# Optimization experiments

Hardware: AMD Instinct MI355X
Metric: run time of the kernel (lower is better)

Reference implementation:

```python
import jax, jax.numpy as jnp
import numpy as np

N_NODES = 50000
N_EDGES = 800000
D_IN = 128
D_OUT = 128


def setup_inputs() -> dict:
    key = jax.random.key(0)
    k_feat, k_src, k_dst, k_ws, k_bs, k_wn = jax.random.split(key, 6)
    feat = jax.random.normal(k_feat, (N_NODES, D_IN), dtype=jnp.float32)
    src = jax.random.randint(k_src, (N_EDGES,), 0, N_NODES, dtype=jnp.int64)
    dst = jax.random.randint(k_dst, (N_EDGES,), 0, N_NODES, dtype=jnp.int64)
    # fc_self: Linear(D_IN, D_OUT, bias=True); fc_neigh: Linear(D_IN, D_OUT, bias=False)
    W_self = jax.random.normal(k_ws, (D_OUT, D_IN), dtype=jnp.float32) * (1.0 / np.sqrt(D_IN))
    b_self = jax.random.normal(k_bs, (D_OUT,), dtype=jnp.float32) * 0.01
    # xavier_uniform with relu gain
    gain = float(np.sqrt(2.0))
    bound = gain * float(np.sqrt(6.0 / (D_IN + D_OUT)))
    W_neigh = jax.random.uniform(k_wn, (D_OUT, D_IN), dtype=jnp.float32, minval=-bound, maxval=bound)
    bias = jnp.zeros((D_OUT,), dtype=jnp.float32)
    return {"feat": feat, "src": src, "dst": dst, "W_self": W_self,
            "b_self": b_self, "W_neigh": W_neigh, "bias": bias}


def reference(feat, src, dst, W_self, b_self, W_neigh, bias):
    # copy_u('h','m') + fn.mean('m','neigh'): gather src feats, mean-reduce by dst.
    # lin_before_mp is False (in_feats == out_feats), so aggregate raw feats first.
    n = feat.shape[0]
    msgs = feat[src]                                             # [E, D_IN]
    neigh_sum = jax.ops.segment_sum(msgs, dst, num_segments=n)   # [N, D_IN]
    deg = jax.ops.segment_sum(jnp.ones(src.shape, feat.dtype), dst, num_segments=n)
    # DGL mean yields 0 for zero-in-degree nodes
    h_neigh = jnp.where(deg[:, None] > 0, neigh_sum / jnp.maximum(deg, 1.0)[:, None], 0.0)
    h_neigh = h_neigh @ W_neigh.T                                # fc_neigh (no bias)
    h_self = feat @ W_self.T + b_self                            # fc_self
    return h_self + h_neigh + bias
```

## Files before the change

kernel.cpp:

```cpp
#include <hip/hip_runtime.h>
#include <hip/hip_fp8.h>

#define N_NODES 50000
#define N_EDGES 800000
#define D 128
#define NBUK 782
#define CAPB 1344
#define SRTN (CAPB + 64*7)
#define EPB 2048
#define SCAT_BLOCKS 391
#define FEAT_BLOCKS 3125
#define W_BLOCKS 32
#define CAPC 16

typedef __bf16 bf16x8 __attribute__((ext_vector_type(8)));
typedef __bf16 bf16x4 __attribute__((ext_vector_type(4)));
typedef float  f32x4  __attribute__((ext_vector_type(4)));
typedef float  f32x2  __attribute__((ext_vector_type(2)));

#if defined(__has_builtin)
#if __has_builtin(__builtin_amdgcn_cvt_pk_f32_fp8) && __has_builtin(__builtin_amdgcn_cvt_pk_fp8_f32)
#define HW_FP8 1
#endif
#endif

#define OFF_PACKED 0ull
#define OFF_FEAT8  19568768ull
#define OFF_WC16   25968896ull
#define OFF_BIASC  26034432ull

__device__ __forceinline__ float fp8tof_sw(unsigned char b) {
    __hip_fp8_e4m3 t; t.__x = b;
    return (float)t;
}

__global__ __launch_bounds__(256)
void prep_kernel(const int* __restrict__ src, const int* __restrict__ dst,
                 int* __restrict__ packed,
                 const float* __restrict__ feat, unsigned char* __restrict__ feat8,
                 const float* __restrict__ Ws, const float* __restrict__ Wn,
                 const float* __restrict__ b_self, const float* __restrict__ bias,
                 __bf16* __restrict__ Wc16, float* __restrict__ biasc, int n) {
    const int tid = threadIdx.x;
    const int bid = blockIdx.x;
    if (bid < SCAT_BLOCKS) {
        __shared__ int hist[NBUK];
        __shared__ int boff[NBUK];
        __shared__ int srtL[EPB];
        __shared__ int wtot[4];
        const int e0 = bid * EPB;
        int d[8], s[8];
        for (int i = tid; i < NBUK; i += 256) hist[i] = 0;
        __syncthreads();
        #pragma unroll
        for (int j = 0; j < 8; ++j) {
            int e = e0 + j * 256 + tid;
            bool ok = e < n;
            d[j] = ok ? dst[e] : -1;
            s[j] = ok ? src[e] : 0;
            if (ok) atomicAdd(&hist[d[j] >> 6], 1);
        }
        __syncthreads();
        {
            const int lane = tid & 63;
            const int wv = tid >> 6;
            const int b4 = tid * 4;
            int h0 = (b4 + 0 < NBUK) ? hist[b4 + 0] : 0;
            int h1 = (b4 + 1 < NBUK) ? hist[b4 + 1] : 0;
            int h2 = (b4 + 2 < NBUK) ? hist[b4 + 2] : 0;
            int h3 = (b4 + 3 < NBUK) ? hist[b4 + 3] : 0;
            int sm = h0 + h1 + h2 + h3;
            int v = sm;
            #pragma unroll
            for (int o = 1; o < 64; o <<= 1) {
                int u = __shfl_up(v, o);
                if (lane >= o) v += u;
            }
            if (lane == 63) wtot[wv] = v;
            __syncthreads();
            if (tid == 0) {
                int r = 0;
                #pragma unroll
                for (int j = 0; j < 4; ++j) { int t = wtot[j]; wtot[j] = r; r += t; }
            }
            __syncthreads();
            int ex = wtot[wv] + v - sm;
            if (b4 + 0 < NBUK) { boff[b4 + 0] = ex;                hist[b4 + 0] = 0; }
            if (b4 + 1 < NBUK) { boff[b4 + 1] = ex + h0;           hist[b4 + 1] = 0; }
            if (b4 + 2 < NBUK) { boff[b4 + 2] = ex + h0 + h1;      hist[b4 + 2] = 0; }
            if (b4 + 3 < NBUK) { boff[b4 + 3] = ex + h0 + h1 + h2; hist[b4 + 3] = 0; }
        }
        __syncthreads();
        #pragma unroll
        for (int j = 0; j < 8; ++j) {
            if (d[j] >= 0) {
                int bk = d[j] >> 6;
                int r = atomicAdd(&hist[bk], 1);
                srtL[boff[bk] + r] = ((d[j] & 63) << 16) | s[j];
            }
        }
        __syncthreads();
        for (int idx = tid; idx < NBUK * 4; idx += 256) {
            int bk = idx >> 2;
            int q4 = (idx & 3) * 4;
            int off = boff[bk];
            int c = hist[bk];
            int4 v;
            v.x = (q4 + 0 < c) ? srtL[off + q4 + 0] : -1;
            v.y = (q4 + 1 < c) ? srtL[off + q4 + 1] : -1;
            v.z = (q4 + 2 < c) ? srtL[off + q4 + 2] : -1;
            v.w = (q4 + 3 < c) ? srtL[off + q4 + 3] : -1;
            *(int4*)&packed[((size_t)bk * SCAT_BLOCKS + bid) * CAPC + q4] = v;
        }
    } else if (bid < SCAT_BLOCKS + FEAT_BLOCKS) {
        size_t i = ((size_t)(bid - SCAT_BLOCKS) * 256 + tid) * 8;
        float4 f0 = *(const float4*)(feat + i);
        float4 f1 = *(const float4*)(feat + i + 4);
#ifdef HW_FP8
        int q0 = __builtin_amdgcn_cvt_pk_fp8_f32(f0.x, f0.y, 0, false);
        q0     = __builtin_amdgcn_cvt_pk_fp8_f32(f0.z, f0.w, q0, true);
        int q1 = __builtin_amdgcn_cvt_pk_fp8_f32(f1.x, f1.y, 0, false);
        q1     = __builtin_amdgcn_cvt_pk_fp8_f32(f1.z, f1.w, q1, true);
        uint2 qq; qq.x = (unsigned)q0; qq.y = (unsigned)q1;
        *(uint2*)(feat8 + i) = qq;
#else
        float fv[8] = {f0.x, f0.y, f0.z, f0.w, f1.x, f1.y, f1.z, f1.w};
        union { unsigned char b[8]; unsigned long long u; } q;
        #pragma unroll
        for (int j = 0; j < 8; ++j) { __hip_fp8_e4m3 e(fv[j]); q.b[j] = e.__x; }
        *(unsigned long long*)(feat8 + i) = q.u;
#endif
    } else if (bid < SCAT_BLOCKS + FEAT_BLOCKS + W_BLOCKS) {
        int idx = (bid - SCAT_BLOCKS - FEAT_BLOCKS) * 256 + tid;
        int col = idx >> 6;
        int kq  = (idx & 63) * 4;
        const float* srcp = (kq < D) ? (Ws + (size_t)col * D + kq)
                                     : (Wn + (size_t)col * D + (kq - D));
        float4 f = *(const float4*)srcp;
        bf16x4 t;
        t[0]=(__bf16)f.x; t[1]=(__bf16)f.y; t[2]=(__bf16)f.z; t[3]=(__bf16)f.w;
        *(bf16x4*)(Wc16 + (size_t)col * 256 + kq) = t;
    } else {
        if (tid < D) biasc[tid] = b_self[tid] + bias[tid];
        else if (tid < D + 32)
            ((unsigned*)(feat8 + (size_t)N_NODES * D))[tid - 128] = 0u;
    }
}

__global__ __launch_bounds__(512)
void fused_kernel(const float* __restrict__ feat,
                  const unsigned char* __restrict__ feat8,
                  const int* __restrict__ packed,
                  const __bf16* __restrict__ Wc16,
                  const float* __restrict__ biasc,
                  float* __restrict__ out) {
    __shared__ __bf16 At[64][264];
    __shared__ int pk[CAPB];
    __shared__ int srt[SRTN];
    __shared__ int cnt[64];
    __shared__ int loff[64];
    __shared__ int degs[64];
    __shared__ int nv;
    const int tid = threadIdx.x;
    const int b = blockIdx.x;
    const int node0 = b * 64;

    if (tid == 0) nv = 0;
    if (tid < 64) cnt[tid] = 0;
    __syncthreads();

    {
        const int4* sp = (const int4*)(packed + (size_t)b * SCAT_BLOCKS * CAPC);
        for (int i = tid; i < SCAT_BLOCKS * 4; i += 512) {
            int4 v = sp[i];
            if (v.x != -1) { int p = atomicAdd(&nv, 1); if (p < CAPB) pk[p] = v.x; }
            if (v.y != -1) { int p = atomicAdd(&nv, 1); if (p < CAPB) pk[p] = v.y; }
            if (v.z != -1) { int p = atomicAdd(&nv, 1); if (p < CAPB) pk[p] = v.z; }
            if (v.w != -1) { int p = atomicAdd(&nv, 1); if (p < CAPB) pk[p] = v.w; }
        }
    }

    for (int idx = tid; idx < 1024; idx += 512) {
        int row = idx >> 4;
        int seg = (idx & 15) * 8;
        int nn = node0 + row;
        bf16x8 t = {};
        if (nn < N_NODES) {
            const float* fp = feat + (size_t)nn * D + seg;
            float4 f0 = *(const float4*)fp;
            float4 f1 = *(const float4*)(fp + 4);
            t[0]=(__bf16)f0.x; t[1]=(__bf16)f0.y; t[2]=(__bf16)f0.z; t[3]=(__bf16)f0.w;
            t[4]=(__bf16)f1.x; t[5]=(__bf16)f1.y; t[6]=(__bf16)f1.z; t[7]=(__bf16)f1.w;
        }
        *(bf16x8*)&At[row][seg] = t;
    }
    __syncthreads();
    const int ecnt = min(nv, CAPB);

    for (int i = tid; i < ecnt; i += 512) atomicAdd(&cnt[pk[i] >> 16], 1);
    __syncthreads();
    if (tid < 64) {
        int c = cnt[tid];
        int cp = (c + 7) & ~7;
        int v = cp;
        #pragma unroll
        for (int o = 1; o < 64; o <<= 1) {
            int u = __shfl_up(v, o);
            if (tid >= o) v += u;
        }
        loff[tid] = v - cp;
        degs[tid] = c;
        cnt[tid] = 0;
    }
    __syncthreads();
    for (int i = tid; i < ecnt; i += 512) {
        int p = pk[i];
        int l = p >> 16;
        int r = atomicAdd(&cnt[l], 1);
        srt[loff[l] + r] = p & 0xFFFF;
    }
    if (tid < 64) {
        int c = degs[tid];
        int cp = (c + 7) & ~7;
        int base0 = loff[tid];
        for (int j = c; j < cp; ++j) srt[base0 + j] = N_NODES;
    }
    __syncthreads();

    {
        const int hw = tid >> 5;
        const int lane = tid & 31;
        const unsigned int* g8 = (const unsigned int*)feat8;
        #pragma unroll
        for (int t = 0; t < 4; ++t) {
            int i = hw + t * 16;
            int dg = degs[i];
            int dgp = (dg + 7) & ~7;
            const int base0 = loff[i];
            float a0 = 0.f, a1 = 0.f, a2 = 0.f, a3 = 0.f;
            for (int j = 0; j < dgp; j += 8) {
                int s[8]; unsigned int w[8];
                #pragma unroll
                for (int q = 0; q < 8; ++q) s[q] = srt[base0 + j + q];
                #pragma unroll
                for (int q = 0; q < 8; ++q)
                    w[q] = g8[(size_t)s[q] * 32 + lane];
                #pragma unroll
                for (int q = 0; q < 8; ++q) {
#ifdef HW_FP8
                    f32x2 lo = __builtin_amdgcn_cvt_pk_f32_fp8((int)w[q], false);
                    f32x2 hi = __builtin_amdgcn_cvt_pk_f32_fp8((int)w[q], true);
                    a0 += lo[0]; a1 += lo[1]; a2 += hi[0]; a3 += hi[1];
#else
                    a0 += fp8tof_sw(w[q] & 0xFF);
                    a1 += fp8tof_sw((w[q] >> 8) & 0xFF);
                    a2 += fp8tof_sw((w[q] >> 16) & 0xFF);
                    a3 += fp8tof_sw(w[q] >> 24);
#endif
                }
            }
            float sc = dg > 0 ? 1.0f / (float)dg : 0.f;
            bf16x4 hv;
            hv[0] = (__bf16)(a0 * sc); hv[1] = (__bf16)(a1 * sc);
            hv[2] = (__bf16)(a2 * sc); hv[3] = (__bf16)(a3 * sc);
            *(bf16x4*)&At[i][128 + lane * 4] = hv;
        }
    }
    __syncthreads();

    const int wv = tid >> 6;
    const int lane = tid & 63;
    const int m = lane & 15;
    const int quad = lane >> 4;
    const int r0 = (wv & 1) * 32;
    const int c0 = (wv >> 1) * 32;

    f32x4 acc[2][2] = {};
    #pragma unroll
    for (int k0 = 0; k0 < 256; k0 += 32) {
        const int kk = k0 + quad * 8;
        bf16x8 a0 = *(const bf16x8*)&At[r0 + m][kk];
        bf16x8 a1 = *(const bf16x8*)&At[r0 + 16 + m][kk];
        #pragma unroll
        for (int ct = 0; ct < 2; ++ct) {
            int col = c0 + ct * 16 + m;
            bf16x8 bb = *(const bf16x8*)(Wc16 + (size_t)col * 256 + kk);
            acc[0][ct] = __builtin_amdgcn_mfma_f32_16x16x32_bf16(a0, bb, acc[0][ct], 0, 0, 0);
            acc[1][ct] = __builtin_amdgcn_mfma_f32_16x16x32_bf16(a1, bb, acc[1][ct], 0, 0, 0);
        }
    }
    __syncthreads();

    float* Ct = (float*)&At[0][0];
    #pragma unroll
    for (int rt = 0; rt < 2; ++rt) {
        #pragma unroll
        for (int ct = 0; ct < 2; ++ct) {
            int ccol = c0 + ct * 16 + m;
            int crow = r0 + rt * 16 + quad * 4;
            #pragma unroll
            for (int r = 0; r < 4; ++r)
                Ct[(crow + r) * 132 + ccol] = acc[rt][ct][r];
        }
    }
    __syncthreads();
    for (int idx = tid; idx < 64 * 32; idx += 512) {
        int row = idx >> 5;
        int c4 = (idx & 31) * 4;
        int nn = node0 + row;
        if (nn < N_NODES) {
            float4 v = *(float4*)&Ct[row * 132 + c4];
            float4 bb = *(const float4*)(biasc + c4);
            v.x += bb.x; v.y += bb.y; v.z += bb.z; v.w += bb.w;
            *(float4*)&out[(size_t)nn * D + c4] = v;
        }
    }
}

extern "C" void kernel_launch(void* const* d_in, const int* in_sizes, int n_in,
                              void* d_out, int out_size, void* d_ws, size_t ws_size,
                              hipStream_t stream) {
    const float* feat    = (const float*)d_in[0];
    const int*   src     = (const int*)d_in[1];
    const int*   dst     = (const int*)d_in[2];
    const float* W_self  = (const float*)d_in[3];
    const float* b_self  = (const float*)d_in[4];
    const float* W_neigh = (const float*)d_in[5];
    const float* bias    = (const float*)d_in[6];
    float* out = (float*)d_out;
    char*  ws  = (char*)d_ws;

    int* packed  = (int*)(ws + OFF_PACKED);
    unsigned char* feat8 = (unsigned char*)(ws + OFF_FEAT8);
    __bf16* Wc16  = (__bf16*)(ws + OFF_WC16);
    float*  biasc = (float*)(ws + OFF_BIASC);
    const int n_edges = in_sizes[1];

    prep_kernel<<<dim3(SCAT_BLOCKS + FEAT_BLOCKS + W_BLOCKS + 1), 256, 0, stream>>>(
        src, dst, packed, feat, feat8, W_self, W_neigh, b_self, bias,
        Wc16, biasc, n_edges);
    fused_kernel<<<dim3(NBUK), 512, 0, stream>>>(
        feat, feat8, packed, Wc16, biasc, out);
}
```

Baseline: 136.2 us.

## Alias edge staging buffer with A tile, compact edges via wave scan, prefetch self features

The edge staging buffer now shares LDS with the bf16 A tile, and the sorted source indices are stored as 16-bit values, which shrinks the block's shared memory and may allow more resident blocks per CU. Edge compaction replaces one LDS atomic per edge with a wave prefix scan plus one atomic per wave, and the per-node degree count is folded into the same pass, removing a loop and a barrier. Self-feature rows are loaded into registers at kernel start and written to LDS only after the sort, so the global load latency overlaps the edge bucketing. In exchange the kernel holds more live registers during the sort phase.

Measured after the change: 131.0 us. -3.8%, faster.

```diff
diff --git a/kernel.cpp b/kernel.cpp
--- a/kernel.cpp
+++ b/kernel.cpp
@@ -154,16 +154,34 @@
                   const __bf16* __restrict__ Wc16,
                   const float* __restrict__ biasc,
                   float* __restrict__ out) {
-    __shared__ __bf16 At[64][264];
-    __shared__ int pk[CAPB];
-    __shared__ int srt[SRTN];
+    __shared__ __align__(16) char smem[64 * 264 * 2];
+    __shared__ unsigned short srt[SRTN];
     __shared__ int cnt[64];
     __shared__ int loff[64];
     __shared__ int degs[64];
     __shared__ int nv;
+    __bf16 (*At)[264] = (__bf16 (*)[264])smem;
+    int* pk = (int*)smem;
     const int tid = threadIdx.x;
     const int b = blockIdx.x;
     const int node0 = b * 64;
+    const int lane64 = tid & 63;
+
+    const int srow = tid >> 3;
+    const int scol = (tid & 7) * 16;
+    const int snn = node0 + srow;
+    bf16x8 st0 = {}, st1 = {};
+    if (snn < N_NODES) {
+        const float* fp = feat + (size_t)snn * D + scol;
+        float4 f0 = *(const float4*)(fp);
+        float4 f1 = *(const float4*)(fp + 4);
+        float4 f2 = *(const float4*)(fp + 8);
+        float4 f3 = *(const float4*)(fp + 12);
+        st0[0]=(__bf16)f0.x; st0[1]=(__bf16)f0.y; st0[2]=(__bf16)f0.z; st0[3]=(__bf16)f0.w;
+        st0[4]=(__bf16)f1.x; st0[5]=(__bf16)f1.y; st0[6]=(__bf16)f1.z; st0[7]=(__bf16)f1.w;
+        st1[0]=(__bf16)f2.x; st1[1]=(__bf16)f2.y; st1[2]=(__bf16)f2.z; st1[3]=(__bf16)f2.w;
+        st1[4]=(__bf16)f3.x; st1[5]=(__bf16)f3.y; st1[6]=(__bf16)f3.z; st1[7]=(__bf16)f3.w;
+    }
 
     if (tid == 0) nv = 0;
     if (tid < 64) cnt[tid] = 0;
@@ -171,34 +189,32 @@
 
     {
         const int4* sp = (const int4*)(packed + (size_t)b * SCAT_BLOCKS * CAPC);
-        for (int i = tid; i < SCAT_BLOCKS * 4; i += 512) {
-            int4 v = sp[i];
-            if (v.x != -1) { int p = atomicAdd(&nv, 1); if (p < CAPB) pk[p] = v.x; }
-            if (v.y != -1) { int p = atomicAdd(&nv, 1); if (p < CAPB) pk[p] = v.y; }
-            if (v.z != -1) { int p = atomicAdd(&nv, 1); if (p < CAPB) pk[p] = v.z; }
-            if (v.w != -1) { int p = atomicAdd(&nv, 1); if (p < CAPB) pk[p] = v.w; }
-        }
-    }
-
-    for (int idx = tid; idx < 1024; idx += 512) {
-        int row = idx >> 4;
-        int seg = (idx & 15) * 8;
-        int nn = node0 + row;
-        bf16x8 t = {};
-        if (nn < N_NODES) {
-            const float* fp = feat + (size_t)nn * D + seg;
-            float4 f0 = *(const float4*)fp;
-            float4 f1 = *(const float4*)(fp + 4);
-            t[0]=(__bf16)f0.x; t[1]=(__bf16)f0.y; t[2]=(__bf16)f0.z; t[3]=(__bf16)f0.w;
-            t[4]=(__bf16)f1.x; t[5]=(__bf16)f1.y; t[6]=(__bf16)f1.z; t[7]=(__bf16)f1.w;
-        }
-        *(bf16x8*)&At[row][seg] = t;
+        #pragma unroll
+        for (int k = 0; k < 4; ++k) {
+            int i = k * 512 + tid;
+            int4 v; v.x = -1; v.y = -1; v.z = -1; v.w = -1;
+            if (i < SCAT_BLOCKS * 4) v = sp[i];
+            int c = (v.x != -1) + (v.y != -1) + (v.z != -1) + (v.w != -1);
+            int p = c;
+            #pragma unroll
+            for (int o = 1; o < 64; o <<= 1) {
+                int u = __shfl_up(p, o);
+                if (lane64 >= o) p += u;
+            }
+            int wt = __shfl(p, 63);
+            int wb = 0;
+            if (lane64 == 63 && wt) wb = atomicAdd(&nv, wt);
+            wb = __shfl(wb, 63);
+            int pos = wb + p - c;
+            if (v.x != -1) { if (pos < CAPB) { pk[pos] = v.x; atomicAdd(&cnt[v.x >> 16], 1); } ++pos; }
+            if (v.y != -1) { if (pos < CAPB) { pk[pos] = v.y; atomicAdd(&cnt[v.y >> 16], 1); } ++pos; }
+            if (v.z != -1) { if (pos < CAPB) { pk[pos] = v.z; atomicAdd(&cnt[v.z >> 16], 1); } ++pos; }
+            if (v.w != -1) { if (pos < CAPB) { pk[pos] = v.w; atomicAdd(&cnt[v.w >> 16], 1); } ++pos; }
+        }
     }
     __syncthreads();
     const int ecnt = min(nv, CAPB);
 
-    for (int i = tid; i < ecnt; i += 512) atomicAdd(&cnt[pk[i] >> 16], 1);
-    __syncthreads();
     if (tid < 64) {
         int c = cnt[tid];
         int cp = (c + 7) & ~7;
@@ -217,15 +233,18 @@
         int p = pk[i];
         int l = p >> 16;
         int r = atomicAdd(&cnt[l], 1);
-        srt[loff[l] + r] = p & 0xFFFF;
+        srt[loff[l] + r] = (unsigned short)p;
     }
     if (tid < 64) {
         int c = degs[tid];
         int cp = (c + 7) & ~7;
         int base0 = loff[tid];
-        for (int j = c; j < cp; ++j) srt[base0 + j] = N_NODES;
-    }
-    __syncthreads();
+        for (int j = c; j < cp; ++j) srt[base0 + j] = (unsigned short)N_NODES;
+    }
+    __syncthreads();
+
+    *(bf16x8*)&At[srow][scol] = st0;
+    *(bf16x8*)&At[srow][scol + 8] = st1;
 
     {
         const int hw = tid >> 5;
@@ -269,9 +288,8 @@
     __syncthreads();
 
     const int wv = tid >> 6;
-    const int lane = tid & 63;
-    const int m = lane & 15;
-    const int quad = lane >> 4;
+    const int m = lane64 & 15;
+    const int quad = lane64 >> 4;
     const int r0 = (wv & 1) * 32;
     const int c0 = (wv >> 1) * 32;
 
@@ -291,7 +309,7 @@
     }
     __syncthreads();
 
-    float* Ct = (float*)&At[0][0];
+    float* Ct = (float*)smem;
     #pragma unroll
     for (int rt = 0; rt < 2; ++rt) {
         #pragma unroll
```

## Precompute bf16 features, drop LDS edge compaction, write output directly from MFMA registers

Applied to the files above, without the earlier changes.

The prep kernel now also writes a bf16 copy of the features, so the fused kernel loads its self rows as bf16 (half the bytes) and issues that load early, before the synchronisation. The atomic compaction of edges into an LDS pk array is removed. Each thread keeps its packed int4 entries in registers for both the histogram pass and the scatter pass, and the sorted-edge array shrinks to 16-bit entries. The epilogue drops the LDS staging and its two barriers and stores accumulators directly with bias, at the cost of uncoalesced scalar global stores and an extra 12.8 MB bf16 write in prep.

New measurement: 129.0 us. -5.3%, faster.

```diff
diff --git a/kernel.cpp b/kernel.cpp
--- a/kernel.cpp
+++ b/kernel.cpp
@@ -28,6 +28,7 @@
 #define OFF_FEAT8  19568768ull
 #define OFF_WC16   25968896ull
 #define OFF_BIASC  26034432ull
+#define OFF_FEAT16 26035200ull
 
 __device__ __forceinline__ float fp8tof_sw(unsigned char b) {
     __hip_fp8_e4m3 t; t.__x = b;
@@ -38,6 +39,7 @@
 void prep_kernel(const int* __restrict__ src, const int* __restrict__ dst,
                  int* __restrict__ packed,
                  const float* __restrict__ feat, unsigned char* __restrict__ feat8,
+                 __bf16* __restrict__ feat16,
                  const float* __restrict__ Ws, const float* __restrict__ Wn,
                  const float* __restrict__ b_self, const float* __restrict__ bias,
                  __bf16* __restrict__ Wc16, float* __restrict__ biasc, int n) {
@@ -116,6 +118,10 @@
         size_t i = ((size_t)(bid - SCAT_BLOCKS) * 256 + tid) * 8;
         float4 f0 = *(const float4*)(feat + i);
         float4 f1 = *(const float4*)(feat + i + 4);
+        bf16x8 t16;
+        t16[0]=(__bf16)f0.x; t16[1]=(__bf16)f0.y; t16[2]=(__bf16)f0.z; t16[3]=(__bf16)f0.w;
+        t16[4]=(__bf16)f1.x; t16[5]=(__bf16)f1.y; t16[6]=(__bf16)f1.z; t16[7]=(__bf16)f1.w;
+        *(bf16x8*)(feat16 + i) = t16;
 #ifdef HW_FP8
         int q0 = __builtin_amdgcn_cvt_pk_fp8_f32(f0.x, f0.y, 0, false);
         q0     = __builtin_amdgcn_cvt_pk_fp8_f32(f0.z, f0.w, q0, true);
@@ -148,57 +154,53 @@
 }
 
 __global__ __launch_bounds__(512)
-void fused_kernel(const float* __restrict__ feat,
+void fused_kernel(const __bf16* __restrict__ feat16,
                   const unsigned char* __restrict__ feat8,
                   const int* __restrict__ packed,
                   const __bf16* __restrict__ Wc16,
                   const float* __restrict__ biasc,
                   float* __restrict__ out) {
     __shared__ __bf16 At[64][264];
-    __shared__ int pk[CAPB];
-    __shared__ int srt[SRTN];
+    __shared__ unsigned short srt[SRTN];
     __shared__ int cnt[64];
     __shared__ int loff[64];
     __shared__ int degs[64];
-    __shared__ int nv;
     const int tid = threadIdx.x;
     const int b = blockIdx.x;
     const int node0 = b * 64;
 
-    if (tid == 0) nv = 0;
+    const int srow = tid >> 3;
+    const int scol = (tid & 7) * 16;
+    const int snn = node0 + srow;
+    bf16x8 st0 = {}, st1 = {};
+    if (snn < N_NODES) {
+        const __bf16* sp = feat16 + (size_t)snn * D + scol;
+        st0 = *(const bf16x8*)sp;
+        st1 = *(const bf16x8*)(sp + 8);
+    }
+
     if (tid < 64) cnt[tid] = 0;
     __syncthreads();
 
+    int4 vv0, vv1, vv2, vv3;
     {
         const int4* sp = (const int4*)(packed + (size_t)b * SCAT_BLOCKS * CAPC);
-        for (int i = tid; i < SCAT_BLOCKS * 4; i += 512) {
-            int4 v = sp[i];
-            if (v.x != -1) { int p = atomicAdd(&nv, 1); if (p < CAPB) pk[p] = v.x; }
-            if (v.y != -1) { int p = atomicAdd(&nv, 1); if (p < CAPB) pk[p] = v.y; }
-            if (v.z != -1) { int p = atomicAdd(&nv, 1); if (p < CAPB) pk[p] = v.z; }
-            if (v.w != -1) { int p = atomicAdd(&nv, 1); if (p < CAPB) pk[p] = v.w; }
-        }
-    }
-
-    for (int idx = tid; idx < 1024; idx += 512) {
-        int row = idx >> 4;
-        int seg = (idx & 15) * 8;
-        int nn = node0 + row;
-        bf16x8 t = {};
-        if (nn < N_NODES) {
-            const float* fp = feat + (size_t)nn * D + seg;
-            float4 f0 = *(const float4*)fp;
-            float4 f1 = *(const float4*)(fp + 4);
-            t[0]=(__bf16)f0.x; t[1]=(__bf16)f0.y; t[2]=(__bf16)f0.z; t[3]=(__bf16)f0.w;
-            t[4]=(__bf16)f1.x; t[5]=(__bf16)f1.y; t[6]=(__bf16)f1.z; t[7]=(__bf16)f1.w;
-        }
-        *(bf16x8*)&At[row][seg] = t;
-    }
-    __syncthreads();
-    const int ecnt = min(nv, CAPB);
-
-    for (int i = tid; i < ecnt; i += 512) atomicAdd(&cnt[pk[i] >> 16], 1);
-    __syncthreads();
+        int4 none; none.x = -1; none.y = -1; none.z = -1; none.w = -1;
+        int i0 = tid, i1 = 512 + tid, i2 = 1024 + tid, i3 = 1536 + tid;
+        vv0 = sp[i0];
+        vv1 = sp[i1];
+        vv2 = (i2 < SCAT_BLOCKS * 4) ? sp[i2] : none;
+        vv3 = (i3 < SCAT_BLOCKS * 4) ? sp[i3] : none;
+        #define HISTV(v) do { \
+            if ((v).x != -1) atomicAdd(&cnt[(v).x >> 16], 1); \
+            if ((v).y != -1) atomicAdd(&cnt[(v).y >> 16], 1); \
+            if ((v).z != -1) atomicAdd(&cnt[(v).z >> 16], 1); \
+            if ((v).w != -1) atomicAdd(&cnt[(v).w >> 16], 1); } while (0)
+        HISTV(vv0); HISTV(vv1); HISTV(vv2); HISTV(vv3);
+        #undef HISTV
+    }
+    __syncthreads();
+
     if (tid < 64) {
         int c = cnt[tid];
         int cp = (c + 7) & ~7;
@@ -213,17 +215,24 @@
         cnt[tid] = 0;
     }
     __syncthreads();
-    for (int i = tid; i < ecnt; i += 512) {
-        int p = pk[i];
-        int l = p >> 16;
-        int r = atomicAdd(&cnt[l], 1);
-        srt[loff[l] + r] = p & 0xFFFF;
+
+    *(bf16x8*)&At[srow][scol] = st0;
+    *(bf16x8*)&At[srow][scol + 8] = st1;
+    {
+        #define SCATV(v) do { \
+            if ((v).x != -1) { int l = (v).x >> 16; int r = atomicAdd(&cnt[l], 1); int o = loff[l] + r; if (o < SRTN) srt[o] = (unsigned short)(v).x; } \
+            if ((v).y != -1) { int l = (v).y >> 16; int r = atomicAdd(&cnt[l], 1); int o = loff[l] + r; if (o < SRTN) srt[o] = (unsigned short)(v).y; } \
+            if ((v).z != -1) { int l = (v).z >> 16; int r = atomicAdd(&cnt[l], 1); int o = loff[l] + r; if (o < SRTN) srt[o] = (unsigned short)(v).z; } \
+            if ((v).w != -1) { int l = (v).w >> 16; int r = atomicAdd(&cnt[l], 1); int o = loff[l] + r; if (o < SRTN) srt[o] = (unsigned short)(v).w; } } while (0)
+        SCATV(vv0); SCATV(vv1); SCATV(vv2); SCATV(vv3);
+        #undef SCATV
     }
     if (tid < 64) {
         int c = degs[tid];
         int cp = (c + 7) & ~7;
         int base0 = loff[tid];
-        for (int j = c; j < cp; ++j) srt[base0 + j] = N_NODES;
+        for (int j = c; j < cp; ++j)
+            if (base0 + j < SRTN) srt[base0 + j] = (unsigned short)N_NODES;
     }
     __syncthreads();
 
@@ -289,30 +298,20 @@
             acc[1][ct] = __builtin_amdgcn_mfma_f32_16x16x32_bf16(a1, bb, acc[1][ct], 0, 0, 0);
         }
     }
-    __syncthreads();
-
-    float* Ct = (float*)&At[0][0];
+
     #pragma unroll
-    for (int rt = 0; rt < 2; ++rt) {
-        #pragma unroll
-        for (int ct = 0; ct < 2; ++ct) {
-            int ccol = c0 + ct * 16 + m;
-            int crow = r0 + rt * 16 + quad * 4;
+    for (int ct = 0; ct < 2; ++ct) {
+        int col = c0 + ct * 16 + m;
+        float bb = biasc[col];
+        #pragma unroll
+        for (int rt = 0; rt < 2; ++rt) {
+            int rowb = node0 + r0 + rt * 16 + quad * 4;
             #pragma unroll
-            for (int r = 0; r < 4; ++r)
-                Ct[(crow + r) * 132 + ccol] = acc[rt][ct][r];
-        }
-    }
-    __syncthreads();
-    for (int idx = tid; idx < 64 * 32; idx += 512) {
-        int row = idx >> 5;
-        int c4 = (idx & 31) * 4;
-        int nn = node0 + row;
-        if (nn < N_NODES) {
-            float4 v = *(float4*)&Ct[row * 132 + c4];
-            float4 bb = *(const float4*)(biasc + c4);
-            v.x += bb.x; v.y += bb.y; v.z += bb.z; v.w += bb.w;
-            *(float4*)&out[(size_t)nn * D + c4] = v;
+            for (int r = 0; r < 4; ++r) {
+                int nn = rowb + r;
+                if (nn < N_NODES)
+                    out[(size_t)nn * D + col] = acc[rt][ct][r] + bb;
+            }
         }
     }
 }
@@ -332,13 +331,14 @@
 
     int* packed  = (int*)(ws + OFF_PACKED);
     unsigned char* feat8 = (unsigned char*)(ws + OFF_FEAT8);
-    __bf16* Wc16  = (__bf16*)(ws + OFF_WC16);
-    float*  biasc = (float*)(ws + OFF_BIASC);
+    __bf16* Wc16   = (__bf16*)(ws + OFF_WC16);
+    float*  biasc  = (float*)(ws + OFF_BIASC);
+    __bf16* feat16 = (__bf16*)(ws + OFF_FEAT16);
     const int n_edges = in_sizes[1];
 
     prep_kernel<<<dim3(SCAT_BLOCKS + FEAT_BLOCKS + W_BLOCKS + 1), 256, 0, stream>>>(
-        src, dst, packed, feat, feat8, W_self, W_neigh, b_self, bias,
+        src, dst, packed, feat, feat8, feat16, W_self, W_neigh, b_self, bias,
         Wc16, biasc, n_edges);
     fused_kernel<<<dim3(NBUK), 512, 0, stream>>>(
-        feat, feat8, packed, Wc16, biasc, out);
+        feat16, feat8, packed, Wc16, biasc, out);
 }
```
